# Performance work log

Hardware: AMD Instinct MI355X
Metric: run time of the kernel (lower is better)

The kernel has to match this reference:

```python
import jax, jax.numpy as jnp
import numpy as np

D = 192      # model dim (out_channels)
DIN = 384    # d_inner = 2*D
N = 16       # d_state
DTR = 12     # dt_rank = ceil(D/16)
K = 4        # depthwise conv kernel size
NB = 3       # total mamba blocks (2 stacked + 1 in downsample)


def setup_inputs() -> dict:
    key = jax.random.key(0)
    ks = jax.random.split(key, 8)
    rn = lambda k, shape, s: jax.random.normal(k, shape, jnp.float32) * s
    inp = {
        "x": jax.random.normal(ks[0], (2, 96, 56, 56), jnp.float32),
        "proj_w": rn(ks[1], (D, 96), 0.1),
        "proj_b": jnp.zeros((D,), jnp.float32),
        "bn_g": jnp.ones((D,), jnp.float32),
        "bn_b": jnp.zeros((D,), jnp.float32),
        "bn_mean": jnp.zeros((D,), jnp.float32),
        "bn_var": jnp.ones((D,), jnp.float32),
        "ln_g": jnp.ones((NB, D), jnp.float32),
        "ln_b": jnp.zeros((NB, D), jnp.float32),
        "Win": rn(ks[2], (NB, 2 * DIN, D), 0.05),
        "b_in": jnp.zeros((NB, 2 * DIN), jnp.float32),
        "conv_w": rn(ks[3], (NB, DIN, K), 0.2),
        "conv_b": jnp.zeros((NB, DIN), jnp.float32),
        "Wx": rn(ks[4], (NB, DTR + 2 * N, DIN), 0.05),
        "Wdt": rn(ks[5], (NB, DIN, DTR), 0.05),
        "bdt": jnp.full((NB, DIN), -4.6, jnp.float32),  # softplus ~ 0.01
        "A_log": jnp.log(jnp.broadcast_to(jnp.arange(1, N + 1, dtype=jnp.float32), (NB, DIN, N))),
        "Dskip": jnp.ones((NB, DIN), jnp.float32),
        "Wout": rn(ks[6], (NB, D, DIN), 0.05),
        "bout": jnp.zeros((NB, D), jnp.float32),
    }
    return inp


def _mamba(x, ln_g, ln_b, Win, b_in, conv_w, conv_b, Wx, Wdt, bdt, A_log, Dskip, Wout, bout):
    # x: (B, C, H, W) -> flatten spatial dims to a sequence (B, L, C)
    B, C, H, W = x.shape
    L = H * W
    seq = x.reshape(B, C, L).transpose(0, 2, 1)
    mu = seq.mean(-1, keepdims=True)
    var = seq.var(-1, keepdims=True)
    h = (seq - mu) * jax.lax.rsqrt(var + 1e-5) * ln_g + ln_b  # LayerNorm
    xz = jnp.einsum('bld,ed->ble', h, Win) + b_in              # (B, L, 2*DIN)
    xi, z = jnp.split(xz, 2, axis=-1)
    # depthwise causal conv1d along L
    xc = jnp.pad(xi.transpose(0, 2, 1), ((0, 0), (0, 0), (K - 1, 0)))
    xc = jax.lax.conv_general_dilated(xc, conv_w[:, None, :], (1,), 'VALID',
                                      feature_group_count=DIN) + conv_b[:, None]
    xi = jax.nn.silu(xc).transpose(0, 2, 1)                    # (B, L, DIN)
    proj = jnp.einsum('ble,pe->blp', xi, Wx)                   # (B, L, DTR+2N)
    dtl = proj[..., :DTR]
    Bm = proj[..., DTR:DTR + N]
    Cm = proj[..., DTR + N:]
    dt = jax.nn.softplus(jnp.einsum('blr,er->ble', dtl, Wdt) + bdt)  # (B, L, DIN)
    A = -jnp.exp(A_log)                                         # (DIN, N)
    dA = jnp.exp(dt[..., None] * A)                             # (B, L, DIN, N)
    dBx = (dt * xi)[..., None] * Bm[:, :, None, :]              # (B, L, DIN, N)

    def step(hc, t):
        dA_t, dBx_t, C_t = t
        hc = dA_t * hc + dBx_t                                  # (B, DIN, N)
        return hc, jnp.einsum('ben,bn->be', hc, C_t)

    h0 = jnp.zeros((B, DIN, N), x.dtype)
    _, ys = jax.lax.scan(step, h0, (dA.transpose(1, 0, 2, 3),
                                    dBx.transpose(1, 0, 2, 3),
                                    Cm.transpose(1, 0, 2)))
    y = ys.transpose(1, 0, 2) + Dskip * xi
    y = y * jax.nn.silu(z)
    out = jnp.einsum('ble,de->bld', y, Wout) + bout
    return out.transpose(0, 2, 1).reshape(B, C, H, W)


def _maxpool2(x):
    return jax.lax.reduce_window(x, -jnp.inf, jax.lax.max,
                                 (1, 1, 2, 2), (1, 1, 2, 2), 'VALID')


def reference(x, proj_w, proj_b, bn_g, bn_b, bn_mean, bn_var, ln_g, ln_b, Win, b_in,
              conv_w, conv_b, Wx, Wdt, bdt, A_log, Dskip, Wout, bout):
    # proj (conv1x1) + BatchNorm (eval-mode running stats)
    x = jnp.einsum('bchw,oc->bohw', x, proj_w) + proj_b[:, None, None]
    x = (x - bn_mean[:, None, None]) * jax.lax.rsqrt(bn_var[:, None, None] + 1e-5) \
        * bn_g[:, None, None] + bn_b[:, None, None]
    blk = lambda i, v: _mamba(v, ln_g[i], ln_b[i], Win[i], b_in[i], conv_w[i], conv_b[i],
                              Wx[i], Wdt[i], bdt[i], A_log[i], Dskip[i], Wout[i], bout[i])
    for i in range(2):  # residual mamba blocks
        x = x + blk(i, x)
    skip = x
    x = blk(2, _maxpool2(x))  # downsample: maxpool then mamba (no residual)
    return (x, skip)
```

## Files before the change

### kernel.cpp

```cpp
#include <hip/hip_runtime.h>

typedef __attribute__((ext_vector_type(8))) __bf16 bf16x8;
typedef __attribute__((ext_vector_type(4))) __bf16 bf16x4;
typedef __attribute__((ext_vector_type(4))) float f32x4;

#define DEV static __device__ __forceinline__

DEV float fast_rcp(float x) { return __builtin_amdgcn_rcpf(x); }
DEV float sigm(float x) { return fast_rcp(1.f + __expf(-x)); }
DEV float siluf(float x) { return x * sigm(x); }
DEV float softplusf(float x) { return x > 20.f ? x : __logf(1.f + __expf(x)); }

__global__ __launch_bounds__(256) void k_proj_wcvt(
    const float* __restrict__ x, const float* __restrict__ pw,
    const float* __restrict__ pb, const float* __restrict__ bng,
    const float* __restrict__ bnb, const float* __restrict__ bnm,
    const float* __restrict__ bnv, float* __restrict__ v,
    const float* __restrict__ Win, const float* __restrict__ Wout,
    const float* __restrict__ Wx, __bf16* __restrict__ Wb)
{
  constexpr int SAP = 104;
  __shared__ __bf16 As[64 * SAP];
  __shared__ __bf16 Ws[64 * SAP];
  const int tid = threadIdx.x;
  const int bid = blockIdx.x;

  if (bid >= 294) {
    const int idx = (bid - 294) * 256 + tid;
    if (idx < 442368) Wb[idx] = (__bf16)Win[idx];
    else if (idx < 663552) Wb[idx] = (__bf16)Wout[idx - 442368];
    else Wb[idx] = (__bf16)Wx[idx - 663552];
    return;
  }

  const int r0 = (bid % 98) * 64;
  const int col0 = (bid / 98) * 64;
  const int b = r0 / 3136, l0 = r0 % 3136;
  const int lane = tid & 63, wv = tid >> 6;
  const int rh = wv >> 1, ch = wv & 1;
  const int lm = lane & 15, quad = lane >> 4;

#pragma unroll
  for (int it = 0; it < 6; ++it) {
    const int idx = tid + it * 256;
    const int c = idx >> 4, l4 = idx & 15;
    const float4 t = *(const float4*)(x + ((size_t)(b * 96 + c)) * 3136 + l0 + l4 * 4);
    As[(l4 * 4 + 0) * SAP + c] = (__bf16)t.x;
    As[(l4 * 4 + 1) * SAP + c] = (__bf16)t.y;
    As[(l4 * 4 + 2) * SAP + c] = (__bf16)t.z;
    As[(l4 * 4 + 3) * SAP + c] = (__bf16)t.w;
  }
#pragma unroll
  for (int it = 0; it < 6; ++it) {
    const int idx = tid + it * 256;
    const int wr = idx / 24, kc = (idx % 24) * 4;
    const float4 t = *(const float4*)(pw + (size_t)(col0 + wr) * 96 + kc);
    bf16x4 o;
    o[0] = (__bf16)t.x; o[1] = (__bf16)t.y; o[2] = (__bf16)t.z; o[3] = (__bf16)t.w;
    *(bf16x4*)(&Ws[wr * SAP + kc]) = o;
  }
  __syncthreads();

  f32x4 acc[2][2] = {};
#pragma unroll
  for (int ks = 0; ks < 3; ++ks) {
    const int kb = ks * 32 + quad * 8;
    bf16x8 a0 = *(const bf16x8*)(&As[(rh * 32 + lm) * SAP + kb]);
    bf16x8 a1 = *(const bf16x8*)(&As[(rh * 32 + 16 + lm) * SAP + kb]);
    bf16x8 b0 = *(const bf16x8*)(&Ws[(ch * 32 + lm) * SAP + kb]);
    bf16x8 b1 = *(const bf16x8*)(&Ws[(ch * 32 + 16 + lm) * SAP + kb]);
    acc[0][0] = __builtin_amdgcn_mfma_f32_16x16x32_bf16(a0, b0, acc[0][0], 0, 0, 0);
    acc[0][1] = __builtin_amdgcn_mfma_f32_16x16x32_bf16(a0, b1, acc[0][1], 0, 0, 0);
    acc[1][0] = __builtin_amdgcn_mfma_f32_16x16x32_bf16(a1, b0, acc[1][0], 0, 0, 0);
    acc[1][1] = __builtin_amdgcn_mfma_f32_16x16x32_bf16(a1, b1, acc[1][1], 0, 0, 0);
  }

#pragma unroll
  for (int ti = 0; ti < 2; ++ti)
#pragma unroll
    for (int tj = 0; tj < 2; ++tj) {
      const int gcol = col0 + ch * 32 + tj * 16 + lm;
      const float s = rsqrtf(bnv[gcol] + 1e-5f) * bng[gcol];
      const float sh = (pb[gcol] - bnm[gcol]) * s + bnb[gcol];
#pragma unroll
      for (int j = 0; j < 4; ++j) {
        const int grow = r0 + rh * 32 + ti * 16 + quad * 4 + j;
        v[(size_t)grow * 192 + gcol] = acc[ti][tj][j] * s + sh;
      }
    }
}

__global__ __launch_bounds__(256) void k_conv(
    const float* __restrict__ xz, __bf16* __restrict__ xiB,
    const float* __restrict__ cw, const float* __restrict__ cb,
    int Lseq, int nthreads)
{
  const int idx = blockIdx.x * 256 + threadIdx.x;
  if (idx >= nthreads) return;
  const int e = idx % 384;
  const int seg = idx / 384;
  const int nseg = Lseq / 8;
  const int b = seg / nseg;
  const int l0 = (seg % nseg) * 8;
  const float4 w4 = *(const float4*)(cw + e * 4);
  const float bv = cb[e];
  float xv[11];
#pragma unroll
  for (int k = 0; k < 11; ++k) {
    const int l = l0 - 3 + k;
    xv[k] = (l >= 0) ? xz[(size_t)(b * Lseq + l) * 768 + e] : 0.f;
  }
#pragma unroll
  for (int j = 0; j < 8; ++j) {
    const float a = bv + xv[j] * w4.x + xv[j + 1] * w4.y + xv[j + 2] * w4.z + xv[j + 3] * w4.w;
    xiB[(size_t)(b * Lseq + l0 + j) * 384 + e] = (__bf16)siluf(a);
  }
}

constexpr int EPI_XZ = 0, EPI_G2 = 1, EPI_RES = 2, EPI_RES_SKIP = 3, EPI_OUT2 = 4;

template <int AMODE, int NT, int EPI>
__global__ __launch_bounds__(256) void k_gemm(
    const void* __restrict__ Ain, const __bf16* __restrict__ W,
    const float* __restrict__ bias, float* __restrict__ O,
    int M, int K, int Nvalid,
    float* __restrict__ dtlbuf, float* __restrict__ bcbuf,
    float* __restrict__ oflt,
    const float* __restrict__ lng, const float* __restrict__ lnb,
    int Lseq)
{
  constexpr int SA = 200;
  constexpr int CT = (NT == 1) ? 2 : 4;
  __shared__ __bf16 As[64 * SA];
  __shared__ __bf16 Ws[64 * NT * SA];
  __shared__ float lnS[(AMODE >= 2) ? 384 : 1];
  const int tid = threadIdx.x;
  const int r0 = blockIdx.x * 64;
  const int col0 = blockIdx.y * (64 * NT);
  const int lane = tid & 63, wv = tid >> 6;
  const int rh = (NT == 1) ? (wv >> 1) : (wv & 1);
  const int ch = (NT == 1) ? (wv & 1) : (wv >> 1);
  const int lm = lane & 15, quad = lane >> 4;

  if constexpr (AMODE >= 2) {
    if (tid < 192) { lnS[tid] = lng[tid]; lnS[192 + tid] = lnb[tid]; }
    __syncthreads();
  }

  f32x4 acc[2][CT] = {};
  const int nkp = K / 192;
  for (int kp = 0; kp < nkp; ++kp) {
    if (kp) __syncthreads();
    if constexpr (AMODE == 1) {
      const __bf16* Ab = (const __bf16*)Ain;
#pragma unroll
      for (int it = 0; it < 6; ++it) {
        const int idx = tid + it * 256;
        const int row = idx / 24, kc = (idx % 24) * 8;
        const int gr = min(r0 + row, M - 1);
        bf16x8 val = *(const bf16x8*)(Ab + (size_t)gr * K + kp * 192 + kc);
        *(bf16x8*)(&As[row * SA + kc]) = val;
      }
    } else {
      const float* A = (const float*)Ain;
      const int row = tid >> 2, part = tid & 3;
      const int gr = min(r0 + row, M - 1);
      const int cbase = part * 48;
      float4 tv[12];
      if constexpr (AMODE == 2) {
#pragma unroll
        for (int j = 0; j < 12; ++j)
          tv[j] = *(const float4*)(A + (size_t)gr * 192 + cbase + j * 4);
      } else {
        const int bb = gr / 784, l2 = gr % 784;
        const int h2 = l2 / 28, w2 = l2 % 28;
        const float* p0 = A + (size_t)(bb * 3136 + h2 * 112 + w2 * 2) * 192;
#pragma unroll
        for (int j = 0; j < 12; ++j) {
          const int cc = cbase + j * 4;
          const float4 a0 = *(const float4*)(p0 + cc);
          const float4 a1 = *(const float4*)(p0 + 192 + cc);
          const float4 a2 = *(const float4*)(p0 + 56 * 192 + cc);
          const float4 a3 = *(const float4*)(p0 + 57 * 192 + cc);
          tv[j].x = fmaxf(fmaxf(a0.x, a1.x), fmaxf(a2.x, a3.x));
          tv[j].y = fmaxf(fmaxf(a0.y, a1.y), fmaxf(a2.y, a3.y));
          tv[j].z = fmaxf(fmaxf(a0.z, a1.z), fmaxf(a2.z, a3.z));
          tv[j].w = fmaxf(fmaxf(a0.w, a1.w), fmaxf(a2.w, a3.w));
        }
      }
      float s = 0.f, sq = 0.f;
#pragma unroll
      for (int j = 0; j < 12; ++j) {
        s += tv[j].x + tv[j].y + tv[j].z + tv[j].w;
        sq += tv[j].x * tv[j].x + tv[j].y * tv[j].y + tv[j].z * tv[j].z + tv[j].w * tv[j].w;
      }
      s += __shfl_xor(s, 1); s += __shfl_xor(s, 2);
      sq += __shfl_xor(sq, 1); sq += __shfl_xor(sq, 2);
      const float mean = s * (1.f / 192.f);
      const float rstd = rsqrtf(sq * (1.f / 192.f) - mean * mean + 1e-5f);
#pragma unroll
      for (int j = 0; j < 12; ++j) {
        const int c = cbase + j * 4;
        bf16x4 o;
        o[0] = (__bf16)((tv[j].x - mean) * rstd * lnS[c + 0] + lnS[192 + c + 0]);
        o[1] = (__bf16)((tv[j].y - mean) * rstd * lnS[c + 1] + lnS[192 + c + 1]);
        o[2] = (__bf16)((tv[j].z - mean) * rstd * lnS[c + 2] + lnS[192 + c + 2]);
        o[3] = (__bf16)((tv[j].w - mean) * rstd * lnS[c + 3] + lnS[192 + c + 3]);
        *(bf16x4*)(&As[row * SA + c]) = o;
      }
    }
#pragma unroll
    for (int it = 0; it < 6 * NT; ++it) {
      const int idx = tid + it * 256;
      const int wr = idx / 24, kc = (idx % 24) * 8;
      const int gw = col0 + wr;
      bf16x8 val = {};
      if (gw < Nvalid) val = *(const bf16x8*)(W + (size_t)gw * K + kp * 192 + kc);
      *(bf16x8*)(&Ws[wr * SA + kc]) = val;
    }
    __syncthreads();
#pragma unroll
    for (int ks = 0; ks < 6; ++ks) {
      const int kb = ks * 32 + quad * 8;
      bf16x8 a0 = *(const bf16x8*)(&As[(rh * 32 + lm) * SA + kb]);
      bf16x8 a1 = *(const bf16x8*)(&As[(rh * 32 + 16 + lm) * SA + kb]);
#pragma unroll
      for (int tj = 0; tj < CT; ++tj) {
        bf16x8 bfr = *(const bf16x8*)(&Ws[(ch * (16 * CT) + tj * 16 + lm) * SA + kb]);
        acc[0][tj] = __builtin_amdgcn_mfma_f32_16x16x32_bf16(a0, bfr, acc[0][tj], 0, 0, 0);
        acc[1][tj] = __builtin_amdgcn_mfma_f32_16x16x32_bf16(a1, bfr, acc[1][tj], 0, 0, 0);
      }
    }
  }

  if constexpr (EPI == EPI_G2) {
    __shared__ float dtlS[64 * 12];
#pragma unroll
    for (int ti = 0; ti < 2; ++ti)
#pragma unroll
      for (int tj = 0; tj < CT; ++tj) {
        const int colt = ch * (16 * CT) + tj * 16 + lm;
#pragma unroll
        for (int j = 0; j < 4; ++j) {
          const int rowt = rh * 32 + ti * 16 + quad * 4 + j;
          const int grow = r0 + rowt;
          const float val = acc[ti][tj][j];
          if (colt < 12) dtlS[rowt * 12 + colt] = val;
          else if (colt < 44 && grow < M)
            bcbuf[(size_t)grow * 32 + (colt - 12)] = val;
        }
      }
    __syncthreads();
    for (int idx = tid; idx < 64 * 12; idx += 256) {
      const int grow = r0 + idx / 12;
      if (grow < M) dtlbuf[(size_t)grow * 12 + idx % 12] = dtlS[idx];
    }
  } else {
#pragma unroll
    for (int ti = 0; ti < 2; ++ti)
#pragma unroll
      for (int tj = 0; tj < CT; ++tj) {
        const int colt = ch * (16 * CT) + tj * 16 + lm;
        const int gcol = col0 + colt;
        const float bv = bias[gcol];
#pragma unroll
        for (int j = 0; j < 4; ++j) {
          const int rowt = rh * 32 + ti * 16 + quad * 4 + j;
          const int grow = r0 + rowt;
          if (grow >= M) continue;
          const float val = acc[ti][tj][j] + bv;
          if constexpr (EPI == EPI_XZ) {
            O[(size_t)grow * 768 + gcol] = val;
          } else if constexpr (EPI == EPI_RES) {
            O[(size_t)grow * 192 + gcol] += val;
          } else if constexpr (EPI == EPI_RES_SKIP) {
            const float nv = O[(size_t)grow * 192 + gcol] + val;
            O[(size_t)grow * 192 + gcol] = nv;
            const int b = grow / 3136, l = grow % 3136;
            oflt[b * 602112 + gcol * 3136 + l] = nv;
          } else {
            const int b = grow / 784, l = grow % 784;
            oflt[b * 150528 + gcol * 784 + l] = val;
          }
        }
      }
  }
}

constexpr int SC_LC = 14, SC_T = 7, SC_TN = 2;

DEV void compute_dts(const float* __restrict__ dtl, const float* __restrict__ Wdt,
                     const float* __restrict__ bdt, int rowbase, int e, int t,
                     float* dtlS, float* wdtS)
{
  for (int idx = t; idx < SC_LC * 12; idx += 128)
    dtlS[idx] = dtl[(size_t)(rowbase + idx / 12) * 12 + idx % 12];
#pragma unroll
  for (int r = 0; r < 12; ++r) wdtS[r * 128 + t] = Wdt[(size_t)e * 12 + r];
}

__global__ __launch_bounds__(128) void k_scan1(
    const float* __restrict__ dtl, const __bf16* __restrict__ xi,
    const float* __restrict__ bc, const float* __restrict__ Wdt,
    const float* __restrict__ bdt, const float* __restrict__ A_log,
    float* __restrict__ P, float* __restrict__ S, int Lseq, int NC)
{
  __shared__ float Bs[SC_LC * 16];
  __shared__ float dts[SC_LC * 128];
  __shared__ float dtlS[SC_LC * 12];
  __shared__ float wdtS[12 * 128];
  const int t = threadIdx.x;
  const int e = blockIdx.y * 128 + t;
  const int c = blockIdx.x % NC;
  const int b = blockIdx.x / NC;
  const int rowbase = b * Lseq + c * SC_LC;

  for (int idx = t; idx < SC_LC * 16; idx += 128) {
    const int l = idx >> 4, q = idx & 15;
    Bs[idx] = bc[(size_t)(rowbase + l) * 32 + q];
  }
  compute_dts(dtl, Wdt, bdt, rowbase, e, t, dtlS, wdtS);
  const float bdte = bdt[e];

  float An2[16];
  {
    const float4* a4 = (const float4*)(A_log + e * 16);
    float4 t0 = a4[0], t1 = a4[1], t2 = a4[2], t3 = a4[3];
    float tmp[16] = {t0.x, t0.y, t0.z, t0.w, t1.x, t1.y, t1.z, t1.w,
                     t2.x, t2.y, t2.z, t2.w, t3.x, t3.y, t3.z, t3.w};
#pragma unroll
    for (int n = 0; n < 16; ++n) An2[n] = -__expf(tmp[n]) * 1.44269504f;
  }
  __syncthreads();
  for (int l = 0; l < SC_LC; ++l) {
    float a = bdte;
#pragma unroll
    for (int r = 0; r < 12; ++r) a += dtlS[l * 12 + r] * wdtS[r * 128 + t];
    dts[l * 128 + t] = softplusf(a);
  }

  float h[16], ap[16];
#pragma unroll
  for (int n = 0; n < 16; ++n) { h[n] = 0.f; ap[n] = 1.f; }

  float xA[SC_T], xB[SC_T];
  auto LOADA = [&](int tt) {
#pragma unroll
    for (int j = 0; j < SC_T; ++j)
      xA[j] = (float)xi[(size_t)(rowbase + tt * SC_T + j) * 384 + e];
  };
  auto LOADB = [&](int tt) {
#pragma unroll
    for (int j = 0; j < SC_T; ++j)
      xB[j] = (float)xi[(size_t)(rowbase + tt * SC_T + j) * 384 + e];
  };
  auto COMP = [&](const float (&x8)[SC_T], int tt) {
#pragma unroll
    for (int j = 0; j < SC_T; ++j) {
      const int l = tt * SC_T + j;
      const float dtv = dts[l * 128 + t];
      const float u = dtv * x8[j];
      const float* Brow = &Bs[l * 16];
#pragma unroll
      for (int n = 0; n < 16; ++n) {
        const float a = __builtin_amdgcn_exp2f(dtv * An2[n]);
        h[n] = a * h[n] + u * Brow[n];
        ap[n] *= a;
      }
    }
  };

  LOADA(0);
#pragma unroll
  for (int tt = 0; tt < SC_TN; ++tt) {
    if (tt & 1) { if (tt + 1 < SC_TN) LOADA(tt + 1); COMP(xB, tt); }
    else        { if (tt + 1 < SC_TN) LOADB(tt + 1); COMP(xA, tt); }
  }

  const size_t o = ((size_t)(b * NC + c) * 384 + e) * 16;
#pragma unroll
  for (int q = 0; q < 4; ++q) {
    *(float4*)(P + o + q * 4) = make_float4(ap[q*4], ap[q*4+1], ap[q*4+2], ap[q*4+3]);
    *(float4*)(S + o + q * 4) = make_float4(h[q*4], h[q*4+1], h[q*4+2], h[q*4+3]);
  }
}

__global__ __launch_bounds__(256) void k_carry(
    const float* __restrict__ P, float* __restrict__ SH, int NC)
{
  const int tid = blockIdx.x * 256 + threadIdx.x;
  const int b = tid / 6144, r = tid % 6144;
  size_t o = (size_t)b * NC * 6144 + r;
  float h = 0.f;
  for (int c0 = 0; c0 < NC; c0 += 4) {
    float p[4], s[4];
#pragma unroll
    for (int k = 0; k < 4; ++k) { p[k] = P[o + (size_t)k * 6144]; s[k] = SH[o + (size_t)k * 6144]; }
#pragma unroll
    for (int k = 0; k < 4; ++k) { SH[o + (size_t)k * 6144] = h; h = p[k] * h + s[k]; }
    o += (size_t)4 * 6144;
  }
}

__global__ __launch_bounds__(128) void k_scan2(
    const float* __restrict__ dtl, const __bf16* __restrict__ xi,
    const float* __restrict__ bc, const float* __restrict__ xz,
    const float* __restrict__ Wdt, const float* __restrict__ bdt,
    const float* __restrict__ A_log, const float* __restrict__ Dskip,
    const float* __restrict__ H0, __bf16* __restrict__ y, int Lseq, int NC)
{
  __shared__ float BCs[SC_LC * 32];
  __shared__ float dts[SC_LC * 128];
  __shared__ float dtlS[SC_LC * 12];
  __shared__ float wdtS[12 * 128];
  const int t = threadIdx.x;
  const int e = blockIdx.y * 128 + t;
  const int c = blockIdx.x % NC;
  const int b = blockIdx.x / NC;
  const int rowbase = b * Lseq + c * SC_LC;

  for (int idx = t; idx < SC_LC * 32; idx += 128)
    BCs[idx] = bc[(size_t)rowbase * 32 + idx];
  compute_dts(dtl, Wdt, bdt, rowbase, e, t, dtlS, wdtS);
  const float bdte = bdt[e];

  float An2[16];
  {
    const float4* a4 = (const float4*)(A_log + e * 16);
    float4 t0 = a4[0], t1 = a4[1], t2 = a4[2], t3 = a4[3];
    float tmp[16] = {t0.x, t0.y, t0.z, t0.w, t1.x, t1.y, t1.z, t1.w,
                     t2.x, t2.y, t2.z, t2.w, t3.x, t3.y, t3.z, t3.w};
#pragma unroll
    for (int n = 0; n < 16; ++n) An2[n] = -__expf(tmp[n]) * 1.44269504f;
  }
  float h[16];
  {
    const size_t o = ((size_t)(b * NC + c) * 384 + e) * 16;
    const float4* h4 = (const float4*)(H0 + o);
    float4 t0 = h4[0], t1 = h4[1], t2 = h4[2], t3 = h4[3];
    h[0]=t0.x; h[1]=t0.y; h[2]=t0.z; h[3]=t0.w;
    h[4]=t1.x; h[5]=t1.y; h[6]=t1.z; h[7]=t1.w;
    h[8]=t2.x; h[9]=t2.y; h[10]=t2.z; h[11]=t2.w;
    h[12]=t3.x; h[13]=t3.y; h[14]=t3.z; h[15]=t3.w;
  }
  __syncthreads();
  for (int l = 0; l < SC_LC; ++l) {
    float a = bdte;
#pragma unroll
    for (int r = 0; r < 12; ++r) a += dtlS[l * 12 + r] * wdtS[r * 128 + t];
    dts[l * 128 + t] = softplusf(a);
  }
  const float Dse = Dskip[e];

  float xA[SC_T], zA[SC_T], xB[SC_T], zB[SC_T];
  auto LOADA = [&](int tt) {
#pragma unroll
    for (int j = 0; j < SC_T; ++j) {
      const size_t r = (size_t)(rowbase + tt * SC_T + j);
      xA[j] = (float)xi[r * 384 + e];
      zA[j] = xz[r * 768 + 384 + e];
    }
  };
  auto LOADB = [&](int tt) {
#pragma unroll
    for (int j = 0; j < SC_T; ++j) {
      const size_t r = (size_t)(rowbase + tt * SC_T + j);
      xB[j] = (float)xi[r * 384 + e];
      zB[j] = xz[r * 768 + 384 + e];
    }
  };
  auto COMP = [&](const float (&x8)[SC_T], const float (&z8)[SC_T], int tt) {
#pragma unroll
    for (int j = 0; j < SC_T; ++j) {
      const int l = tt * SC_T + j;
      const float dtv = dts[l * 128 + t];
      const float xiv = x8[j];
      const float u = dtv * xiv;
      const float* Brow = &BCs[l * 32];
      const float* Crow = Brow + 16;
      float yv = 0.f;
#pragma unroll
      for (int n = 0; n < 16; ++n) {
        const float a = __builtin_amdgcn_exp2f(dtv * An2[n]);
        h[n] = a * h[n] + u * Brow[n];
        yv += h[n] * Crow[n];
      }
      y[(size_t)(rowbase + l) * 384 + e] = (__bf16)((yv + Dse * xiv) * siluf(z8[j]));
    }
  };

  LOADA(0);
#pragma unroll
  for (int tt = 0; tt < SC_TN; ++tt) {
    if (tt & 1) { if (tt + 1 < SC_TN) LOADA(tt + 1); COMP(xB, zB, tt); }
    else        { if (tt + 1 < SC_TN) LOADB(tt + 1); COMP(xA, zA, tt); }
  }
}

extern "C" void kernel_launch(void* const* d_in, const int* in_sizes, int n_in,
                              void* d_out, int out_size, void* d_ws, size_t ws_size,
                              hipStream_t stream)
{
  const float* x    = (const float*)d_in[0];
  const float* pw   = (const float*)d_in[1];
  const float* pb   = (const float*)d_in[2];
  const float* bng  = (const float*)d_in[3];
  const float* bnb  = (const float*)d_in[4];
  const float* bnm  = (const float*)d_in[5];
  const float* bnv  = (const float*)d_in[6];
  const float* lng  = (const float*)d_in[7];
  const float* lnb  = (const float*)d_in[8];
  const float* Win  = (const float*)d_in[9];
  const float* b_in = (const float*)d_in[10];
  const float* cw   = (const float*)d_in[11];
  const float* cb   = (const float*)d_in[12];
  const float* Wx   = (const float*)d_in[13];
  const float* Wdt  = (const float*)d_in[14];
  const float* bdt  = (const float*)d_in[15];
  const float* Alog = (const float*)d_in[16];
  const float* Dsk  = (const float*)d_in[17];
  const float* Wout = (const float*)d_in[18];
  const float* bout = (const float*)d_in[19];

  float* wsf = (float*)d_ws;
  float* v    = wsf;
  float* xz   = v + 1204224;
  float* dtlb = xz + 4816896;
  float* bcb  = dtlb + 75264;
  float* Sb   = bcb + 200704;
  float* Pb   = Sb + 2752512;
  __bf16* xiB = (__bf16*)(Pb + 2752512);
  __bf16* yB  = (__bf16*)(Pb + 2752512 + 1204224);
  __bf16* Wb  = (__bf16*)(Pb + 2752512 + 2408448);

  float* out0 = (float*)d_out;
  float* out1 = out0 + 301056;

  k_proj_wcvt<<<3084, 256, 0, stream>>>(x, pw, pb, bng, bnb, bnm, bnv, v,
                                        Win, Wout, Wx, Wb);

  for (int i = 0; i < 3; ++i) {
    const int big = (i < 2) ? 1 : 0;
    const int Lseq = big ? 3136 : 784;
    const int M = 2 * Lseq;
    const int NC = Lseq / SC_LC;
    const int MB = (M + 63) / 64;
    const float* lng_i = lng + i * 192;
    const float* lnb_i = lnb + i * 192;
    const float* bin_i = b_in + i * 768;
    const float* cw_i  = cw + i * 384 * 4;
    const float* cb_i  = cb + i * 384;
    const float* Wdt_i = Wdt + i * 384 * 12;
    const float* bdt_i = bdt + i * 384;
    const float* Al_i  = Alog + i * 384 * 16;
    const float* Ds_i  = Dsk + i * 384;
    const float* bo_i  = bout + i * 192;
    const __bf16* Winb_i  = Wb + i * 147456;
    const __bf16* Woutb_i = Wb + 442368 + i * 73728;
    const __bf16* Wxb_i   = Wb + 663552 + i * 16896;

    if (big)
      k_gemm<2, 2, EPI_XZ><<<dim3(MB, 6), 256, 0, stream>>>(
          v, Winb_i, bin_i, xz, M, 192, 768,
          nullptr, nullptr, nullptr, lng_i, lnb_i, Lseq);
    else
      k_gemm<3, 2, EPI_XZ><<<dim3(MB, 6), 256, 0, stream>>>(
          v, Winb_i, bin_i, xz, M, 192, 768,
          nullptr, nullptr, nullptr, lng_i, lnb_i, Lseq);
    k_conv<<<(M * 384 / 8 + 255) / 256, 256, 0, stream>>>(
        xz, xiB, cw_i, cb_i, Lseq, M * 384 / 8);
    k_gemm<1, 1, EPI_G2><<<dim3(MB, 1), 256, 0, stream>>>(
        xiB, Wxb_i, nullptr, nullptr, M, 384, 44,
        dtlb, bcb, nullptr, nullptr, nullptr, Lseq);
    k_scan1<<<dim3(2 * NC, 3), 128, 0, stream>>>(
        dtlb, xiB, bcb, Wdt_i, bdt_i, Al_i, Pb, Sb, Lseq, NC);
    k_carry<<<48, 256, 0, stream>>>(Pb, Sb, NC);
    k_scan2<<<dim3(2 * NC, 3), 128, 0, stream>>>(
        dtlb, xiB, bcb, xz, Wdt_i, bdt_i, Al_i, Ds_i, Sb, yB, Lseq, NC);
    if (i == 0)
      k_gemm<1, 1, EPI_RES><<<dim3(MB, 3), 256, 0, stream>>>(
          yB, Woutb_i, bo_i, v, M, 384, 192,
          nullptr, nullptr, nullptr, nullptr, nullptr, Lseq);
    else if (i == 1)
      k_gemm<1, 1, EPI_RES_SKIP><<<dim3(MB, 3), 256, 0, stream>>>(
          yB, Woutb_i, bo_i, v, M, 384, 192,
          nullptr, nullptr, out1, nullptr, nullptr, Lseq);
    else
      k_gemm<1, 1, EPI_OUT2><<<dim3(MB, 3), 256, 0, stream>>>(
          yB, Woutb_i, bo_i, v, M, 384, 192,
          nullptr, nullptr, out0, nullptr, nullptr, Lseq);
  }
}
```

Before: 385.5 us.

## Replace per-chunk decay products with summed dt and recompute decay in carry

```diff
diff --git a/kernel.cpp b/kernel.cpp
--- a/kernel.cpp
+++ b/kernel.cpp
@@ -303,7 +303,7 @@
     const float* __restrict__ dtl, const __bf16* __restrict__ xi,
     const float* __restrict__ bc, const float* __restrict__ Wdt,
     const float* __restrict__ bdt, const float* __restrict__ A_log,
-    float* __restrict__ P, float* __restrict__ S, int Lseq, int NC)
+    float* __restrict__ DT, float* __restrict__ S, int Lseq, int NC)
 {
   __shared__ float Bs[SC_LC * 16];
   __shared__ float dts[SC_LC * 128];
@@ -332,16 +332,19 @@
     for (int n = 0; n < 16; ++n) An2[n] = -__expf(tmp[n]) * 1.44269504f;
   }
   __syncthreads();
+  float dtsum = 0.f;
   for (int l = 0; l < SC_LC; ++l) {
     float a = bdte;
 #pragma unroll
     for (int r = 0; r < 12; ++r) a += dtlS[l * 12 + r] * wdtS[r * 128 + t];
-    dts[l * 128 + t] = softplusf(a);
-  }
-
-  float h[16], ap[16];
-#pragma unroll
-  for (int n = 0; n < 16; ++n) { h[n] = 0.f; ap[n] = 1.f; }
+    const float sp = softplusf(a);
+    dts[l * 128 + t] = sp;
+    dtsum += sp;
+  }
+
+  float h[16];
+#pragma unroll
+  for (int n = 0; n < 16; ++n) h[n] = 0.f;
 
   float xA[SC_T], xB[SC_T];
   auto LOADA = [&](int tt) {
@@ -365,7 +368,6 @@
       for (int n = 0; n < 16; ++n) {
         const float a = __builtin_amdgcn_exp2f(dtv * An2[n]);
         h[n] = a * h[n] + u * Brow[n];
-        ap[n] *= a;
       }
     }
   };
@@ -379,26 +381,49 @@
 
   const size_t o = ((size_t)(b * NC + c) * 384 + e) * 16;
 #pragma unroll
-  for (int q = 0; q < 4; ++q) {
-    *(float4*)(P + o + q * 4) = make_float4(ap[q*4], ap[q*4+1], ap[q*4+2], ap[q*4+3]);
+  for (int q = 0; q < 4; ++q)
     *(float4*)(S + o + q * 4) = make_float4(h[q*4], h[q*4+1], h[q*4+2], h[q*4+3]);
-  }
+  DT[(size_t)(b * NC + c) * 384 + e] = dtsum;
 }
 
 __global__ __launch_bounds__(256) void k_carry(
-    const float* __restrict__ P, float* __restrict__ SH, int NC)
+    const float* __restrict__ DT, float* __restrict__ SH,
+    const float* __restrict__ A_log, int NC)
 {
   const int tid = blockIdx.x * 256 + threadIdx.x;
   const int b = tid / 6144, r = tid % 6144;
-  size_t o = (size_t)b * NC * 6144 + r;
+  const float An2 = -__expf(A_log[r]) * 1.44269504f;
+  const size_t o = (size_t)b * NC * 6144 + r;
+  const size_t od = (size_t)b * NC * 384 + (r >> 4);
+
+  float sA[8], dA[8], sB[8], dB[8];
+  auto LOAD = [&](float (&sv)[8], float (&dv)[8], int c0) {
+#pragma unroll
+    for (int k = 0; k < 8; ++k) {
+      sv[k] = SH[o + (size_t)(c0 + k) * 6144];
+      dv[k] = DT[od + (size_t)(c0 + k) * 384];
+    }
+  };
   float h = 0.f;
-  for (int c0 = 0; c0 < NC; c0 += 4) {
-    float p[4], s[4];
-#pragma unroll
-    for (int k = 0; k < 4; ++k) { p[k] = P[o + (size_t)k * 6144]; s[k] = SH[o + (size_t)k * 6144]; }
-#pragma unroll
-    for (int k = 0; k < 4; ++k) { SH[o + (size_t)k * 6144] = h; h = p[k] * h + s[k]; }
-    o += (size_t)4 * 6144;
+  auto COMP = [&](const float (&sv)[8], const float (&dv)[8], int c0) {
+    float a[8];
+#pragma unroll
+    for (int k = 0; k < 8; ++k) a[k] = __builtin_amdgcn_exp2f(An2 * dv[k]);
+#pragma unroll
+    for (int k = 0; k < 8; ++k) {
+      SH[o + (size_t)(c0 + k) * 6144] = h;
+      h = a[k] * h + sv[k];
+    }
+  };
+
+  LOAD(sA, dA, 0);
+  for (int c0 = 0; c0 < NC; c0 += 16) {
+    if (c0 + 8 < NC) LOAD(sB, dB, c0 + 8);
+    COMP(sA, dA, c0);
+    if (c0 + 8 < NC) {
+      if (c0 + 16 < NC) LOAD(sA, dA, c0 + 16);
+      COMP(sB, dB, c0 + 8);
+    }
   }
 }
 
@@ -574,7 +599,7 @@
         dtlb, bcb, nullptr, nullptr, nullptr, Lseq);
     k_scan1<<<dim3(2 * NC, 3), 128, 0, stream>>>(
         dtlb, xiB, bcb, Wdt_i, bdt_i, Al_i, Pb, Sb, Lseq, NC);
-    k_carry<<<48, 256, 0, stream>>>(Pb, Sb, NC);
+    k_carry<<<48, 256, 0, stream>>>(Pb, Sb, Al_i, NC);
     k_scan2<<<dim3(2 * NC, 3), 128, 0, stream>>>(
         dtlb, xiB, bcb, xz, Wdt_i, bdt_i, Al_i, Ds_i, Sb, yB, Lseq, NC);
     if (i == 0)
```

Measured after the change: 358.4 us. 1.08x faster.
